# Kernel tuning notes

Hardware: AMD Instinct MI355X
Metric: run time of the kernel (lower is better)

Reference implementation:

```python
import jax, jax.numpy as jnp
import numpy as np

N = 50000          # nodes
E = 800000         # edges (avg degree 16)
T = 4              # edge types (edge_attr_dim)
H = 8              # heads
C1 = 16            # state_dim (per-head channels, layer 1)
C2 = 8             # out_dim  (per-head channels, layer 2)
D = 128            # node_attr_dim
NEG = -1e9         # masked-attention logit
LRELU_SLOPE = 0.2  # PyG GATConv default negative_slope


def setup_inputs() -> dict:
    key = jax.random.key(0)
    ks = jax.random.split(key, 12)
    x = jax.random.normal(ks[0], (N, D), jnp.float32)
    edge_src = jax.random.randint(ks[1], (E,), 0, N, jnp.int32)
    edge_dst = jax.random.randint(ks[2], (E,), 0, N, jnp.int32)
    edge_type = jax.random.randint(ks[3], (E,), 0, T, jnp.int32)
    W1 = jax.random.normal(ks[4], (T, D, H * C1), jnp.float32) * (1.0 / np.sqrt(D))
    a1_src = jax.random.normal(ks[5], (T, H, C1), jnp.float32) * 0.1
    a1_dst = jax.random.normal(ks[6], (T, H, C1), jnp.float32) * 0.1
    b1 = jnp.zeros((T, H * C1), jnp.float32)
    W2 = jax.random.normal(ks[7], (T, H * C1, H * C2), jnp.float32) * (1.0 / np.sqrt(H * C1))
    a2_src = jax.random.normal(ks[8], (T, H, C2), jnp.float32) * 0.1
    a2_dst = jax.random.normal(ks[9], (T, H, C2), jnp.float32) * 0.1
    b2 = jnp.zeros((T, H * C2), jnp.float32)
    return dict(x=x, edge_src=edge_src, edge_dst=edge_dst, edge_type=edge_type,
                W1=W1, a1_src=a1_src, a1_dst=a1_dst, b1=b1,
                W2=W2, a2_src=a2_src, a2_dst=a2_dst, b2=b2)


def gat_conv(x_in, W, a_src, a_dst, b, src, dst, mask, n):
    """One PyG-style GATConv (concat heads, eval mode) on masked edge list."""
    heads, c = a_src.shape
    h = (x_in @ W).reshape(n, heads, c)                       # [N,H,C]
    s_src = jnp.sum(h * a_src, axis=-1)                        # [N,H]
    s_dst = jnp.sum(h * a_dst, axis=-1)                        # [N,H]
    e = jax.nn.leaky_relu(s_src[src] + s_dst[dst], LRELU_SLOPE)  # [Et,H]
    e = jnp.where(mask[:, None], e, NEG)
    m = jax.ops.segment_max(e, dst, num_segments=n)            # [N,H]
    p = jnp.exp(e - m[dst]) * mask[:, None].astype(e.dtype)    # unnorm softmax
    denom = jax.ops.segment_sum(p, dst, num_segments=n)        # [N,H]
    msg = p[:, :, None] * h[src]                               # [Et,H,C]
    agg = jax.ops.segment_sum(msg, dst, num_segments=n)        # [N,H,C]
    out = agg / denom[:, :, None]
    return out.reshape(n, heads * c) + b


def reference(x, edge_src, edge_dst, edge_type, W1, a1_src, a1_dst, b1,
              W2, a2_src, a2_dst, b2):
    n = x.shape[0]
    loops = jnp.arange(n, dtype=edge_src.dtype)
    src = jnp.concatenate([edge_src, loops])   # self-loops appended (PyG default)
    dst = jnp.concatenate([edge_dst, loops])
    ones = jnp.ones((n,), bool)
    outs = []
    for t in range(T):
        mask = jnp.concatenate([edge_type == t, ones])
        h1 = gat_conv(x, W1[t], a1_src[t], a1_dst[t], b1[t], src, dst, mask, n)
        h1 = jax.nn.relu(h1)
        h2 = gat_conv(h1, W2[t], a2_src[t], a2_dst[t], b2[t], src, dst, mask, n)
        outs.append(h2)
    return jnp.concatenate(outs, axis=1)       # [N, T*H*C2]
```

## Files before the change

### kernel.cpp

```cpp
#include <hip/hip_runtime.h>
#include <cstddef>

constexpr int NN  = 50000;
constexpr int NE  = 800000;
constexpr int NT  = 4;
constexpr int NH  = 8;
constexpr int C1  = 16;
constexpr int C2  = 8;
constexpr int DD  = 128;
constexpr int HC1 = NH * C1;
constexpr int HC2 = NH * C2;
constexpr int CAP = 22;
constexpr int BSTRIDE = 48;
constexpr float SLOPE = 0.2f;

constexpr int G_ZERO = 2344;
constexpr int G_P1   = NT * 16384 / 256;
constexpr int G_P2   = NT * 8192 / 256;
constexpr int G_SCAT = 782;
constexpr int G_GEMM = (NN + 63) / 64;
constexpr int G_GAT1 = NN / 16;
constexpr int G_GAT2 = (NN + 31) / 32;

using short8 = __attribute__((ext_vector_type(8))) short;
using f32x4  = __attribute__((ext_vector_type(4))) float;
typedef unsigned short u16;
typedef unsigned char  u8;

__device__ __forceinline__ float lrelu(float x) { return x > 0.f ? x : SLOPE * x; }
__device__ __forceinline__ float bfl(unsigned u) { return __uint_as_float(u << 16); }
__device__ __forceinline__ float bfh(unsigned u) { return __uint_as_float(u & 0xffff0000u); }
__device__ __forceinline__ u16 f2bf(float f) {
    unsigned u = __float_as_uint(f);
    return (u16)((u + 0x7fffu + ((u >> 16) & 1u)) >> 16);
}
__device__ __forceinline__ void deci8(uint2 v, float sc, float f[8]) {
    int w0 = (int)v.x, w1 = (int)v.y;
    f[0] = (float)((w0 << 24) >> 24) * sc;
    f[1] = (float)((w0 << 16) >> 24) * sc;
    f[2] = (float)((w0 <<  8) >> 24) * sc;
    f[3] = (float)( w0        >> 24) * sc;
    f[4] = (float)((w1 << 24) >> 24) * sc;
    f[5] = (float)((w1 << 16) >> 24) * sc;
    f[6] = (float)((w1 <<  8) >> 24) * sc;
    f[7] = (float)( w1        >> 24) * sc;
}
__device__ __forceinline__ float dotf(const float h[8], const float* a) {
    return h[0]*a[0] + h[1]*a[1] + h[2]*a[2] + h[3]*a[3]
         + h[4]*a[4] + h[5]*a[5] + h[6]*a[6] + h[7]*a[7];
}
__device__ __forceinline__ float dot8(uint4 hv, const float* a) {
    return bfl(hv.x) * a[0] + bfh(hv.x) * a[1] + bfl(hv.y) * a[2] + bfh(hv.y) * a[3]
         + bfl(hv.z) * a[4] + bfh(hv.z) * a[5] + bfl(hv.w) * a[6] + bfh(hv.w) * a[7];
}

__device__ __forceinline__ void scatter4(int e0, const int* __restrict__ esrc,
        const int* __restrict__ edst, const int* __restrict__ etyp,
        unsigned* __restrict__ bkt, int tmin, int tmax) {
    int bk[4], src[4];
    bool v[4];
    #pragma unroll
    for (int k = 0; k < 4; ++k) {
        int i = e0 + k * 256;
        bk[k] = 0; src[k] = 0;
        v[k] = false;
        if (i < NE) {
            int ty = etyp[i];
            v[k] = (ty >= tmin) && (ty <= tmax);
            if (v[k]) { bk[k] = ty * NN + edst[i]; src[k] = esrc[i]; }
        }
    }
    int slot[4];
    #pragma unroll
    for (int k = 0; k < 4; ++k)
        if (v[k]) slot[k] = atomicAdd((int*)((char*)bkt + (size_t)bk[k] * BSTRIDE), 1);
    #pragma unroll
    for (int k = 0; k < 4; ++k)
        if (v[k] && slot[k] < CAP)
            ((u16*)((char*)bkt + (size_t)bk[k] * BSTRIDE))[2 + slot[k]] = (u16)src[k];
}

__global__ __launch_bounds__(256) void init_kernel(const float* __restrict__ W1,
        u16* __restrict__ wp1, const float* __restrict__ W2, u16* __restrict__ wp2,
        unsigned* __restrict__ bkt) {
    const int b = blockIdx.x, tid = threadIdx.x;
    if (b < G_ZERO) {
        int i = b * 256 + tid;
        if (i < 600000) reinterpret_cast<uint4*>(bkt)[i] = make_uint4(0, 0, 0, 0);
    } else if (b < G_ZERO + G_P1) {
        int i = (b - G_ZERO) * 256 + tid;
        int t = i >> 14, r = i & 16383;
        int ntl = r >> 11, ks = (r >> 9) & 3, lane = (r >> 3) & 63, j = r & 7;
        int col = ntl * 16 + (lane & 15);
        int k   = ks * 32 + (lane >> 4) * 8 + j;
        wp1[i] = f2bf(W1[((size_t)t * DD + k) * HC1 + col]);
    } else {
        int i = (b - G_ZERO - G_P1) * 256 + tid;
        int t = i >> 13, r = i & 8191;
        int ntl = r >> 11, ks = (r >> 9) & 3, lane = (r >> 3) & 63, j = r & 7;
        int col = ntl * 16 + (lane & 15);
        int k   = ks * 32 + (lane >> 4) * 8 + j;
        wp2[i] = f2bf(W2[((size_t)t * HC1 + k) * HC2 + col]);
    }
}

__global__ __launch_bounds__(256) void scat_kernel(const int* __restrict__ esrc,
        const int* __restrict__ edst, const int* __restrict__ etyp,
        unsigned* __restrict__ bkt, int t) {
    scatter4(blockIdx.x * 1024 + threadIdx.x, esrc, edst, etyp, bkt, t, t);
}

__device__ __forceinline__ void gemm1_body(int bx, int tid, const float* __restrict__ x,
        const u16* __restrict__ Wp, u8* __restrict__ h1w, float* __restrict__ scw) {
    constexpr int NTILE = HC1 / 16;
    const int wave = tid >> 6;
    const int lane = tid & 63;
    const int q    = lane >> 4;
    const int c    = lane & 15;
    const int rowbase = bx * 64 + wave * 16;

    int arow = rowbase + c; if (arow >= NN) arow = NN - 1;
    short8 afrag[4];
    const float* xp = x + (size_t)arow * DD + q * 8;
    #pragma unroll
    for (int ks = 0; ks < 4; ++ks) {
        float4 f0 = *reinterpret_cast<const float4*>(xp + ks * 32);
        float4 f1 = *reinterpret_cast<const float4*>(xp + ks * 32 + 4);
        short8 a;
        a[0] = (short)f2bf(f0.x); a[1] = (short)f2bf(f0.y);
        a[2] = (short)f2bf(f0.z); a[3] = (short)f2bf(f0.w);
        a[4] = (short)f2bf(f1.x); a[5] = (short)f2bf(f1.y);
        a[6] = (short)f2bf(f1.z); a[7] = (short)f2bf(f1.w);
        afrag[ks] = a;
    }

    f32x4 acc[NTILE];
    #pragma unroll
    for (int ntl = 0; ntl < NTILE; ++ntl) acc[ntl] = (f32x4){0.f, 0.f, 0.f, 0.f};
    const short8* wp = reinterpret_cast<const short8*>(Wp) + lane;
    #pragma unroll
    for (int ntl = 0; ntl < NTILE; ++ntl)
        #pragma unroll
        for (int ks = 0; ks < 4; ++ks) {
            short8 b = wp[(ntl * 4 + ks) * 64];
            acc[ntl] = __builtin_amdgcn_mfma_f32_16x16x32_bf16(afrag[ks], b, acc[ntl], 0, 0, 0);
        }

    float mx[NTILE][4];
    #pragma unroll
    for (int ntl = 0; ntl < NTILE; ++ntl)
        #pragma unroll
        for (int reg = 0; reg < 4; ++reg) mx[ntl][reg] = fabsf(acc[ntl][reg]);
    #pragma unroll
    for (int m = 1; m < 16; m <<= 1)
        #pragma unroll
        for (int ntl = 0; ntl < NTILE; ++ntl)
            #pragma unroll
            for (int reg = 0; reg < 4; ++reg)
                mx[ntl][reg] = fmaxf(mx[ntl][reg], __shfl_xor(mx[ntl][reg], m));

    #pragma unroll
    for (int ntl = 0; ntl < NTILE; ++ntl)
        #pragma unroll
        for (int reg = 0; reg < 4; ++reg) {
            int row = rowbase + q * 4 + reg;
            if (row < NN) {
                float m = mx[ntl][reg];
                float rs = m > 0.f ? 127.f / m : 0.f;
                int iv = __float2int_rn(acc[ntl][reg] * rs);
                h1w[(size_t)row * HC1 + ntl * 16 + c] = (u8)(char)iv;
            }
        }
    {
        int reg = c >> 2, hp = c & 3;
        int row = rowbase + q * 4 + reg;
        if (row < NN) {
            float2 s;
            s.x = mx[2 * hp][reg] * (1.f / 127.f);
            s.y = mx[2 * hp + 1][reg] * (1.f / 127.f);
            reinterpret_cast<float2*>(scw)[(size_t)row * 4 + hp] = s;
        }
    }
}

__global__ __launch_bounds__(256) void gemm_kernel(const float* __restrict__ x,
        const u16* __restrict__ wp1, u8* __restrict__ h1, float* __restrict__ sc1) {
    int t = blockIdx.x / G_GEMM, bx = blockIdx.x % G_GEMM;
    gemm1_body(bx, threadIdx.x, x, wp1 + (size_t)t * 16384,
               h1 + (size_t)t * NN * HC1, sc1 + (size_t)t * NN * 8);
}

template<int TPN, bool SPLIT, bool I8>
__device__ __forceinline__ void gather_body(const unsigned* __restrict__ bkt, int bk,
        int q, const float* asr, float sdn, const void* __restrict__ hbase,
        const float* __restrict__ scp, float& den, float acc[8]) {
    const uint2* bp = reinterpret_cast<const uint2*>((const char*)bkt + (size_t)bk * BSTRIDE);
    unsigned w[12];
    #pragma unroll
    for (int i = 0; i < 6; ++i) { uint2 u = bp[i]; w[2 * i] = u.x; w[2 * i + 1] = u.y; }
    int deg = (int)w[0]; if (deg > CAP) deg = CAP;
    #pragma unroll
    for (int c = 0; c < 6; ++c) {
        if (c * 4 >= deg) break;
        unsigned lo = w[1 + 2 * c];
        unsigned hi = (c < 5) ? w[2 + 2 * c] : 0u;
        int sv[4] = {(int)(lo & 0xffff), (int)(lo >> 16),
                     (int)(hi & 0xffff), (int)(hi >> 16)};
        #pragma unroll
        for (int j = 0; j < 4; ++j) {
            if (c * 4 + j < deg) {
                int sn = sv[j];
                float hf[8];
                if constexpr (I8) {
                    uint2 hv = reinterpret_cast<const uint2*>(hbase)[(size_t)sn * TPN + q];
                    float sc = scp[(size_t)sn * 8 + (q >> 1)];
                    deci8(hv, sc, hf);
                } else {
                    uint4 hv = reinterpret_cast<const uint4*>(hbase)[(size_t)sn * TPN + q];
                    hf[0] = bfl(hv.x); hf[1] = bfh(hv.x);
                    hf[2] = bfl(hv.y); hf[3] = bfh(hv.y);
                    hf[4] = bfl(hv.z); hf[5] = bfh(hv.z);
                    hf[6] = bfl(hv.w); hf[7] = bfh(hv.w);
                }
                float d = dotf(hf, asr);
                if (SPLIT) d += __shfl_xor(d, 1);
                float pp = __expf(lrelu(d + sdn));
                den += pp;
                #pragma unroll
                for (int i = 0; i < 8; ++i) acc[i] += pp * hf[i];
            }
        }
    }
}

__global__ __launch_bounds__(256) void g1g2_kernel(const unsigned* __restrict__ bkt,
        int t, const u8* __restrict__ h1r, const float* __restrict__ sc1r,
        const float* __restrict__ a1s_t, const float* __restrict__ a1d_t,
        const float* __restrict__ b1t, const u16* __restrict__ wp2t,
        u16* __restrict__ h2w) {
    const int bx = blockIdx.x, tid = threadIdx.x;
    __shared__ u16 lt[16][136];
    const int node0 = bx * 16;
    const int nl    = tid >> 4;
    const int node  = node0 + nl;
    const int q     = tid & 15;
    const int head  = q >> 1;
    const int bk    = t * NN + node;

    float asr[8], adr[8];
    #pragma unroll
    for (int i = 0; i < 8; ++i) {
        asr[i] = a1s_t[head * C1 + (q & 1) * 8 + i];
        adr[i] = a1d_t[head * C1 + (q & 1) * 8 + i];
    }

    uint2 hv = reinterpret_cast<const uint2*>(h1r)[(size_t)node * 16 + q];
    float scn = sc1r[(size_t)node * 8 + head];
    float hs[8];
    deci8(hv, scn, hs);
    float ds = dotf(hs, asr); ds += __shfl_xor(ds, 1);
    float dd = dotf(hs, adr); dd += __shfl_xor(dd, 1);
    const float sdn = dd;

    float p = __expf(lrelu(ds + sdn));
    float den = p;
    float acc[8];
    #pragma unroll
    for (int i = 0; i < 8; ++i) acc[i] = p * hs[i];
    gather_body<16, true, true>(bkt, bk, q, asr, sdn, h1r, sc1r, den, acc);

    float inv = 1.f / den;
    uint4 ov;
    {
        float o[8];
        #pragma unroll
        for (int i = 0; i < 8; ++i)
            o[i] = fmaxf(acc[i] * inv + b1t[q * 8 + i], 0.f);
        ov.x = (unsigned)f2bf(o[0]) | ((unsigned)f2bf(o[1]) << 16);
        ov.y = (unsigned)f2bf(o[2]) | ((unsigned)f2bf(o[3]) << 16);
        ov.z = (unsigned)f2bf(o[4]) | ((unsigned)f2bf(o[5]) << 16);
        ov.w = (unsigned)f2bf(o[6]) | ((unsigned)f2bf(o[7]) << 16);
    }
    *reinterpret_cast<uint4*>(&lt[nl][q * 8]) = ov;
    __syncthreads();

    const int wave = tid >> 6;
    const int lane = tid & 63;
    const int quad = lane >> 4;
    const int c    = lane & 15;
    short8 af[4];
    #pragma unroll
    for (int ks = 0; ks < 4; ++ks)
        af[ks] = *reinterpret_cast<const short8*>(&lt[c][ks * 32 + quad * 8]);
    f32x4 cacc = (f32x4){0.f, 0.f, 0.f, 0.f};
    const short8* wp = reinterpret_cast<const short8*>(wp2t) + lane;
    #pragma unroll
    for (int ks = 0; ks < 4; ++ks)
        cacc = __builtin_amdgcn_mfma_f32_16x16x32_bf16(af[ks], wp[(wave * 4 + ks) * 64], cacc, 0, 0, 0);

    const int col = wave * 16 + c;
    #pragma unroll
    for (int reg = 0; reg < 4; ++reg) {
        int row = node0 + quad * 4 + reg;
        h2w[(size_t)row * HC2 + col] = f2bf(cacc[reg]);
    }
}

__global__ __launch_bounds__(256) void gat2_kernel(const unsigned* __restrict__ bkt,
        int t, const u16* __restrict__ h2r, const float* __restrict__ a2s_t,
        const float* __restrict__ a2d_t, const float* __restrict__ b2t,
        float* __restrict__ out) {
    const int bx = blockIdx.x, tid = threadIdx.x;
    const int node = bx * 32 + (tid >> 3);
    if (node >= NN) return;
    const int q    = tid & 7;
    const int head = q;
    const int bk   = t * NN + node;
    const uint4* __restrict__ h4 = reinterpret_cast<const uint4*>(h2r);

    float asr[8], adr[8];
    #pragma unroll
    for (int i = 0; i < 8; ++i) {
        asr[i] = a2s_t[head * C2 + i];
        adr[i] = a2d_t[head * C2 + i];
    }

    uint4 hv = h4[(size_t)node * 8 + q];
    const float sdn = dot8(hv, adr);
    float p = __expf(lrelu(dot8(hv, asr) + sdn));
    float den = p;
    float acc[8];
    acc[0] = p * bfl(hv.x); acc[1] = p * bfh(hv.x);
    acc[2] = p * bfl(hv.y); acc[3] = p * bfh(hv.y);
    acc[4] = p * bfl(hv.z); acc[5] = p * bfh(hv.z);
    acc[6] = p * bfl(hv.w); acc[7] = p * bfh(hv.w);
    gather_body<8, false, false>(bkt, bk, q, asr, sdn, h2r, nullptr, den, acc);

    float inv = 1.f / den;
    float o[8];
    #pragma unroll
    for (int i = 0; i < 8; ++i) o[i] = acc[i] * inv + b2t[q * 8 + i];
    float* op = out + (size_t)node * (NT * HC2) + t * HC2 + q * 8;
    reinterpret_cast<float4*>(op)[0] = make_float4(o[0], o[1], o[2], o[3]);
    reinterpret_cast<float4*>(op)[1] = make_float4(o[4], o[5], o[6], o[7]);
}

extern "C" void kernel_launch(void* const* d_in, const int* in_sizes, int n_in,
                              void* d_out, int out_size, void* d_ws, size_t ws_size,
                              hipStream_t stream) {
    const float* x    = (const float*)d_in[0];
    const int*   esrc = (const int*)d_in[1];
    const int*   edst = (const int*)d_in[2];
    const int*   etyp = (const int*)d_in[3];
    const float* W1   = (const float*)d_in[4];
    const float* a1s  = (const float*)d_in[5];
    const float* a1d  = (const float*)d_in[6];
    const float* b1   = (const float*)d_in[7];
    const float* W2   = (const float*)d_in[8];
    const float* a2s  = (const float*)d_in[9];
    const float* a2d  = (const float*)d_in[10];
    const float* b2   = (const float*)d_in[11];
    float* out = (float*)d_out;
    char* base = (char*)d_ws;

    u8*    h1  = (u8*)base;
    float* sc1 = (float*)(base + 25600000);
    u16*   h2d[2] = {(u16*)(base + 32000000), (u16*)(base + 38400000)};
    unsigned* bkt = (unsigned*)(base + 44800000);
    u16* wp1 = (u16*)(base + 54400000);
    u16* wp2 = (u16*)(base + 54531072);

    dim3 blk(256);
    hipLaunchKernelGGL(init_kernel, dim3(G_ZERO + G_P1 + G_P2), blk, 0, stream,
                       W1, wp1, W2, wp2, bkt);
    for (int t = 0; t < 4; ++t)
        hipLaunchKernelGGL(scat_kernel, dim3(G_SCAT), blk, 0, stream,
                           esrc, edst, etyp, bkt, t);
    hipLaunchKernelGGL(gemm_kernel, dim3(4 * G_GEMM), blk, 0, stream,
                       x, wp1, h1, sc1);

    auto g1g2 = [&](int t) {
        hipLaunchKernelGGL(g1g2_kernel, dim3(G_GAT1), blk, 0, stream,
                           bkt, t, h1 + (size_t)t * NN * HC1, sc1 + (size_t)t * NN * 8,
                           a1s + t * NH * C1, a1d + t * NH * C1, b1 + t * HC1,
                           wp2 + (size_t)t * 8192, h2d[t & 1]);
    };
    auto gat2 = [&](int t) {
        hipLaunchKernelGGL(gat2_kernel, dim3(G_GAT2), blk, 0, stream,
                           bkt, t, h2d[t & 1], a2s + t * NH * C2, a2d + t * NH * C2,
                           b2 + t * HC2, out);
    };
    g1g2(0); g1g2(1); gat2(0); g1g2(2); gat2(1); g1g2(3); gat2(2); gat2(3);
}
```

Measured before the change: 330.1 us.

## Reuse x fragments across edge types and pack int8 stores via lane permutes

The layer-1 GEMM kernel now launches one block per row tile and loops over all four edge types, so each x tile is loaded and converted to bf16 once rather than four times. The int8 quantized outputs are packed into 32-bit words and redistributed across neighbouring lanes with shuffles and byte permutes, replacing scattered single-byte stores with dword stores. This cuts x read traffic and store transactions, but the grid shrinks by four and each block does four times the work, which may reduce parallelism.

```diff
diff --git a/kernel.cpp b/kernel.cpp
--- a/kernel.cpp
+++ b/kernel.cpp
@@ -52,6 +52,9 @@
 __device__ __forceinline__ float dot8(uint4 hv, const float* a) {
     return bfl(hv.x) * a[0] + bfh(hv.x) * a[1] + bfl(hv.y) * a[2] + bfh(hv.y) * a[3]
          + bfl(hv.z) * a[4] + bfh(hv.z) * a[5] + bfl(hv.w) * a[6] + bfh(hv.w) * a[7];
+}
+__device__ __forceinline__ unsigned qperm(unsigned own, unsigned part, unsigned sel) {
+    return __builtin_amdgcn_perm(own, part, sel);
 }
 
 __device__ __forceinline__ void scatter4(int e0, const int* __restrict__ esrc,
@@ -110,9 +113,10 @@
     scatter4(blockIdx.x * 1024 + threadIdx.x, esrc, edst, etyp, bkt, t, t);
 }
 
-__device__ __forceinline__ void gemm1_body(int bx, int tid, const float* __restrict__ x,
-        const u16* __restrict__ Wp, u8* __restrict__ h1w, float* __restrict__ scw) {
+__global__ __launch_bounds__(256) void gemm_kernel(const float* __restrict__ x,
+        const u16* __restrict__ wp1, u8* __restrict__ h1, float* __restrict__ sc1) {
     constexpr int NTILE = HC1 / 16;
+    const int bx = blockIdx.x, tid = threadIdx.x;
     const int wave = tid >> 6;
     const int lane = tid & 63;
     const int q    = lane >> 4;
@@ -134,60 +138,78 @@
         afrag[ks] = a;
     }
 
-    f32x4 acc[NTILE];
-    #pragma unroll
-    for (int ntl = 0; ntl < NTILE; ++ntl) acc[ntl] = (f32x4){0.f, 0.f, 0.f, 0.f};
-    const short8* wp = reinterpret_cast<const short8*>(Wp) + lane;
-    #pragma unroll
-    for (int ntl = 0; ntl < NTILE; ++ntl)
-        #pragma unroll
-        for (int ks = 0; ks < 4; ++ks) {
-            short8 b = wp[(ntl * 4 + ks) * 64];
-            acc[ntl] = __builtin_amdgcn_mfma_f32_16x16x32_bf16(afrag[ks], b, acc[ntl], 0, 0, 0);
-        }
-
-    float mx[NTILE][4];
-    #pragma unroll
-    for (int ntl = 0; ntl < NTILE; ++ntl)
-        #pragma unroll
-        for (int reg = 0; reg < 4; ++reg) mx[ntl][reg] = fabsf(acc[ntl][reg]);
-    #pragma unroll
-    for (int m = 1; m < 16; m <<= 1)
+    for (int t = 0; t < 4; ++t) {
+        f32x4 acc[NTILE];
+        #pragma unroll
+        for (int ntl = 0; ntl < NTILE; ++ntl) acc[ntl] = (f32x4){0.f, 0.f, 0.f, 0.f};
+        const short8* wp = reinterpret_cast<const short8*>(wp1 + (size_t)t * 16384) + lane;
         #pragma unroll
         for (int ntl = 0; ntl < NTILE; ++ntl)
             #pragma unroll
-            for (int reg = 0; reg < 4; ++reg)
-                mx[ntl][reg] = fmaxf(mx[ntl][reg], __shfl_xor(mx[ntl][reg], m));
-
-    #pragma unroll
-    for (int ntl = 0; ntl < NTILE; ++ntl)
+            for (int ks = 0; ks < 4; ++ks) {
+                short8 b = wp[(ntl * 4 + ks) * 64];
+                acc[ntl] = __builtin_amdgcn_mfma_f32_16x16x32_bf16(afrag[ks], b, acc[ntl], 0, 0, 0);
+            }
+
+        float mx[NTILE][4];
+        #pragma unroll
+        for (int ntl = 0; ntl < NTILE; ++ntl)
+            #pragma unroll
+            for (int reg = 0; reg < 4; ++reg) mx[ntl][reg] = fabsf(acc[ntl][reg]);
+        #pragma unroll
+        for (int m = 1; m < 16; m <<= 1)
+            #pragma unroll
+            for (int ntl = 0; ntl < NTILE; ++ntl)
+                #pragma unroll
+                for (int reg = 0; reg < 4; ++reg)
+                    mx[ntl][reg] = fmaxf(mx[ntl][reg], __shfl_xor(mx[ntl][reg], m));
+
+        u8*    h1w = h1  + (size_t)t * NN * HC1;
+        float* scw = sc1 + (size_t)t * NN * 8;
+
         #pragma unroll
         for (int reg = 0; reg < 4; ++reg) {
             int row = rowbase + q * 4 + reg;
-            if (row < NN) {
+            unsigned w0 = 0, w1 = 0;
+            #pragma unroll
+            for (int ntl = 0; ntl < 4; ++ntl) {
                 float m = mx[ntl][reg];
                 float rs = m > 0.f ? 127.f / m : 0.f;
                 int iv = __float2int_rn(acc[ntl][reg] * rs);
-                h1w[(size_t)row * HC1 + ntl * 16 + c] = (u8)(char)iv;
+                w0 |= ((unsigned)iv & 0xffu) << (8 * ntl);
+            }
+            #pragma unroll
+            for (int ntl = 4; ntl < 8; ++ntl) {
+                float m = mx[ntl][reg];
+                float rs = m > 0.f ? 127.f / m : 0.f;
+                int iv = __float2int_rn(acc[ntl][reg] * rs);
+                w1 |= ((unsigned)iv & 0xffu) << (8 * (ntl - 4));
+            }
+            unsigned sel1 = (c & 1) ? 0x07030501u : 0x02060004u;
+            unsigned p0 = __shfl_xor(w0, 1), p1 = __shfl_xor(w1, 1);
+            w0 = qperm(w0, p0, sel1);
+            w1 = qperm(w1, p1, sel1);
+            unsigned sel2 = (c & 2) ? 0x07060302u : 0x01000504u;
+            p0 = __shfl_xor(w0, 2); p1 = __shfl_xor(w1, 2);
+            w0 = qperm(w0, p0, sel2);
+            w1 = qperm(w1, p1, sel2);
+            if (row < NN) {
+                unsigned* rp = reinterpret_cast<unsigned*>(h1w + (size_t)row * HC1);
+                rp[(c & 3) * 4 + (c >> 2)]       = w0;
+                rp[((c & 3) + 4) * 4 + (c >> 2)] = w1;
             }
         }
-    {
-        int reg = c >> 2, hp = c & 3;
-        int row = rowbase + q * 4 + reg;
-        if (row < NN) {
-            float2 s;
-            s.x = mx[2 * hp][reg] * (1.f / 127.f);
-            s.y = mx[2 * hp + 1][reg] * (1.f / 127.f);
-            reinterpret_cast<float2*>(scw)[(size_t)row * 4 + hp] = s;
+        {
+            int reg = c >> 2, hp = c & 3;
+            int row = rowbase + q * 4 + reg;
+            if (row < NN) {
+                float2 s;
+                s.x = mx[2 * hp][reg] * (1.f / 127.f);
+                s.y = mx[2 * hp + 1][reg] * (1.f / 127.f);
+                reinterpret_cast<float2*>(scw)[(size_t)row * 4 + hp] = s;
+            }
         }
     }
-}
-
-__global__ __launch_bounds__(256) void gemm_kernel(const float* __restrict__ x,
-        const u16* __restrict__ wp1, u8* __restrict__ h1, float* __restrict__ sc1) {
-    int t = blockIdx.x / G_GEMM, bx = blockIdx.x % G_GEMM;
-    gemm1_body(bx, threadIdx.x, x, wp1 + (size_t)t * 16384,
-               h1 + (size_t)t * NN * HC1, sc1 + (size_t)t * NN * 8);
 }
 
 template<int TPN, bool SPLIT, bool I8>
@@ -376,7 +398,7 @@
     for (int t = 0; t < 4; ++t)
         hipLaunchKernelGGL(scat_kernel, dim3(G_SCAT), blk, 0, stream,
                            esrc, edst, etyp, bkt, t);
-    hipLaunchKernelGGL(gemm_kernel, dim3(4 * G_GEMM), blk, 0, stream,
+    hipLaunchKernelGGL(gemm_kernel, dim3(G_GEMM), blk, 0, stream,
                        x, wp1, h1, sc1);
 
     auto g1g2 = [&](int t) {
```

Measured after the change: 320.7 us. 2.8% less time.
